# Kernel optimization log

Measured on AMD Instinct MI355X. Metric: run time of the kernel, lower is better.

The kernel has to match this reference:

```python
import jax, jax.numpy as jnp
import numpy as np

B, T, C, HS = 1024, 128, 384, 64


def setup_inputs() -> dict:
    key = jax.random.key(0)
    k1, k2, k3, k4 = jax.random.split(key, 4)
    std = 1.0 / np.sqrt(C)  # ~ nn.Linear default init scale
    return {
        "x": jax.random.normal(k1, (B, T, C), dtype=jnp.float32),
        "Wq": jax.random.normal(k2, (C, HS), dtype=jnp.float32) * std,
        "Wk": jax.random.normal(k3, (C, HS), dtype=jnp.float32) * std,
        "Wv": jax.random.normal(k4, (C, HS), dtype=jnp.float32) * std,
    }


def reference(x, Wq, Wk, Wv):
    # x: [B, T, C]; Wq/Wk/Wv: [C, HS]
    q = jnp.einsum("btc,ch->bth", x, Wq)
    k = jnp.einsum("btc,ch->bth", x, Wk)
    v = jnp.einsum("btc,ch->bth", x, Wv)
    scale = 1.0 / jnp.sqrt(jnp.asarray(k.shape[-1], dtype=x.dtype))
    wei = jnp.einsum("bth,bsh->bts", q, k) * scale  # [B, T, T]
    t = x.shape[1]
    causal = jnp.tril(jnp.ones((t, t), dtype=bool))
    wei = jnp.where(causal, wei, jnp.asarray(-jnp.inf, dtype=wei.dtype))
    wei = jax.nn.softmax(wei, axis=-1)
    # dropout omitted (eval mode / deterministic reference)
    out = jnp.einsum("bts,bsh->bth", wei, v)  # [B, T, HS]
    return out
```

## Files before the change

### kernel.cpp

```cpp
#include <hip/hip_runtime.h>


typedef __attribute__((ext_vector_type(8)))  short  short8;
typedef __attribute__((ext_vector_type(16))) float  floatx16;
typedef __attribute__((ext_vector_type(4)))  float  float4v;

#define T_DIM   128
#define C_DIM   384
#define HS      64
#define NCHUNK  12
#define SLAB    1536

#define QK_PITCH 68
#define V_PITCH  132
#define P_PITCH  132
#define Q_OFF 0
#define K_OFF 17408
#define V_OFF 34816
#define LDS_BYTES 51712
#define P_OFF 0
#define XS_OFF 0
#define XS_BUF 10240
#define XP    80

#define MFMA(a,b,c) __builtin_amdgcn_mfma_f32_32x32x16_bf16((a),(b),(c),0,0,0)

__device__ inline unsigned short f2bf(float f){
    unsigned u = __builtin_bit_cast(unsigned, f);
    u += 0x7FFFu + ((u >> 16) & 1u);
    return (unsigned short)(u >> 16);
}

__device__ inline short8 ld_b64x2(const char* p){
    union { unsigned long long u[2]; short8 s; } r;
    r.u[0] = *(const unsigned long long*)(p);
    r.u[1] = *(const unsigned long long*)(p + 8);
    return r.s;
}

__global__ void prep_wt(const float* __restrict__ Wq, const float* __restrict__ Wk,
                        const float* __restrict__ Wv, unsigned short* __restrict__ wt){
    int idx = blockIdx.x * 256 + threadIdx.x;
    if (idx >= 48 * SLAB) return;
    int slab = idx / SLAB;
    int rem  = idx - slab * SLAB;
    int n = rem >> 3, j = rem & 7;
    int half = slab & 1, ks = (slab >> 1) & 1, c = slab >> 2;
    int kg = c*32 + ks*16 + half*8 + j;
    const float* W = (n < 64) ? Wq : (n < 128) ? Wk : Wv;
    wt[idx] = f2bf(W[kg * HS + (n & 63)]);
}

__launch_bounds__(256, 2)
__global__ void attn_kernel(const float* __restrict__ x,
                            const unsigned short* __restrict__ wtg,
                            float* __restrict__ out){
    __shared__ __align__(16) char smem[LDS_BYTES];
    const int tid  = threadIdx.x;
    const int lane = tid & 63;
    const int wave = tid >> 6;
    const int l31  = lane & 31;
    const int half = lane >> 5;
    const int koff = half * 8;
    const int b    = blockIdx.x;
    const float* xb = x + (size_t)b * (T_DIM * C_DIM);

    const int mpair = wave & 1;
    const int ntri  = wave >> 1;
    const short8* wf = (const short8*)wtg;
    const int nbase = 96 * ntri + l31;

    const int srow  = tid >> 1;
    const int shalf = tid & 1;
    char* const bw0 = smem + XS_OFF + srow * XP + shalf * 32;

    float4v ldreg[2][4];
    auto xload = [&](int c, int s){
        const float4v* g = (const float4v*)(xb + srow * C_DIM + c * 32 + shalf * 16);
        ldreg[s][0] = g[0]; ldreg[s][1] = g[1];
        ldreg[s][2] = g[2]; ldreg[s][3] = g[3];
    };
    auto cw = [&](int s, int sb){
        short8 o0, o1;
        #pragma unroll
        for (int j = 0; j < 8; ++j){
            o0[j] = (short)f2bf(ldreg[s][j >> 2    ][j & 3]);
            o1[j] = (short)f2bf(ldreg[s][(j >> 2)+2][j & 3]);
        }
        char* p = bw0 + sb * XS_BUF;
        *(short8*)(p)      = o0;
        *(short8*)(p + 16) = o1;
    };

    floatx16 acc[6] = {};
    short8 bfr[2][2][3];

    xload(0, 0);
    xload(1, 1);
    #pragma unroll
    for (int ks = 0; ks < 2; ++ks)
        #pragma unroll
        for (int nbl = 0; nbl < 3; ++nbl)
            bfr[0][ks][nbl] = wf[((0*2 + ks)*2 + half)*192 + nbase + 32*nbl];
    cw(0, 0);
    asm volatile("s_waitcnt lgkmcnt(0)" ::: "memory");
    __builtin_amdgcn_s_barrier();
    asm volatile("" ::: "memory");

    #pragma unroll
    for (int c = 0; c < NCHUNK; ++c){
        if (c + 2 < NCHUNK) xload(c + 2, c & 1);
        if (c + 1 < NCHUNK){
            #pragma unroll
            for (int ks = 0; ks < 2; ++ks)
                #pragma unroll
                for (int nbl = 0; nbl < 3; ++nbl)
                    bfr[(c+1)&1][ks][nbl] =
                        wf[(((c+1)*2 + ks)*2 + half)*192 + nbase + 32*nbl];
        }

        const char* sbuf = smem + XS_OFF + (c & 1) * XS_BUF;
        short8 afr[2][2];
        #pragma unroll
        for (int mbl = 0; mbl < 2; ++mbl){
            const int R = 64*mpair + 32*mbl + l31;
            #pragma unroll
            for (int ks = 0; ks < 2; ++ks)
                afr[ks][mbl] = *(const short8*)(sbuf + R * XP + ks*32 + half*16);
        }
        #pragma unroll
        for (int ks = 0; ks < 2; ++ks)
            #pragma unroll
            for (int nbl = 0; nbl < 3; ++nbl){
                acc[nbl*2+0] = MFMA(afr[ks][0], bfr[c&1][ks][nbl], acc[nbl*2+0]);
                acc[nbl*2+1] = MFMA(afr[ks][1], bfr[c&1][ks][nbl], acc[nbl*2+1]);
            }

        if (c + 1 < NCHUNK){
            cw((c+1)&1, (c+1)&1);
            asm volatile("s_waitcnt lgkmcnt(0)" ::: "memory");
            __builtin_amdgcn_s_barrier();
            asm volatile("" ::: "memory");
        }
    }
    __syncthreads();

    const float QSCALE = 0.125f * 1.44269504088896f;
    #pragma unroll
    for (int nbl = 0; nbl < 3; ++nbl)
        #pragma unroll
        for (int mbl = 0; mbl < 2; ++mbl){
            floatx16 A = acc[nbl*2+mbl];
            int nb = 3*ntri + nbl;
            int mb = 2*mpair + mbl;
            if (nb < 4){
                int base  = (nb < 2) ? Q_OFF : K_OFF;
                int col   = 32 * (nb & 1) + l31;
                float sc  = (nb < 2) ? QSCALE : 1.0f;
                char* bp  = smem + base + col * 2;
                #pragma unroll
                for (int r = 0; r < 16; ++r){
                    int t = 32*mb + (r&3) + 8*(r>>2) + 4*half;
                    *(unsigned short*)(bp + t * (QK_PITCH*2)) = f2bf(A[r] * sc);
                }
            } else {
                int h = 32*(nb-4) + l31;
                char* bp = smem + V_OFF + h * (V_PITCH*2);
                #pragma unroll
                for (int g = 0; g < 4; ++g){
                    int t0 = 32*mb + 8*g + 4*half;
                    union { unsigned short s[4]; unsigned long long u; } pk;
                    pk.s[0]=f2bf(A[4*g+0]); pk.s[1]=f2bf(A[4*g+1]);
                    pk.s[2]=f2bf(A[4*g+2]); pk.s[3]=f2bf(A[4*g+3]);
                    *(unsigned long long*)(bp + t0*2) = pk.u;
                }
            }
        }
    __syncthreads();

    floatx16 accS[4] = {};
    #pragma unroll
    for (int ks = 0; ks < 4; ++ks){
        short8 aq = ld_b64x2(smem + Q_OFF + (32*wave + l31)*(QK_PITCH*2) + (ks*16 + koff)*2);
        #pragma unroll
        for (int st = 0; st < 4; ++st)
            if (st <= wave){
                short8 bk = ld_b64x2(smem + K_OFF + (32*st + l31)*(QK_PITCH*2) + (ks*16 + koff)*2);
                accS[st] = MFMA(aq, bk, accS[st]);
            }
    }
    #pragma unroll
    for (int st = 0; st < 4; ++st)
        if (st <= wave){
            #pragma unroll
            for (int r = 0; r < 16; ++r){
                int trow = (r&3) + 8*(r>>2) + 4*half;
                float e = exp2f(accS[st][r]);
                if (st == wave && l31 > trow) e = 0.0f;
                accS[st][r] = e;
            }
        }

    float linv[16];
    #pragma unroll
    for (int r = 0; r < 16; ++r){
        float l = accS[0][r] + accS[1][r] + accS[2][r] + accS[3][r];
        #pragma unroll
        for (int m = 1; m <= 16; m <<= 1)
            l += __shfl_xor(l, m);
        linv[r] = 1.0f / l;
    }
    __syncthreads();

    #pragma unroll
    for (int st = 0; st < 4; ++st)
        if (st <= wave){
            char* bp = smem + P_OFF + (32*st + l31) * 2;
            #pragma unroll
            for (int r = 0; r < 16; ++r){
                int t = 32*wave + (r&3) + 8*(r>>2) + 4*half;
                *(unsigned short*)(bp + t * (P_PITCH*2)) = f2bf(accS[st][r]);
            }
        }
    __syncthreads();

    floatx16 accO0 = {}, accO1 = {};
    const int nks = 2 * (wave + 1);
    #pragma unroll
    for (int ks = 0; ks < 8; ++ks)
        if (ks < nks){
            short8 ap  = ld_b64x2(smem + P_OFF + (32*wave + l31)*(P_PITCH*2) + (ks*16 + koff)*2);
            short8 bv0 = ld_b64x2(smem + V_OFF + l31        *(V_PITCH*2) + (ks*16 + koff)*2);
            short8 bv1 = ld_b64x2(smem + V_OFF + (l31 + 32) *(V_PITCH*2) + (ks*16 + koff)*2);
            accO0 = MFMA(ap, bv0, accO0);
            accO1 = MFMA(ap, bv1, accO1);
        }

    float* ob = out + (size_t)b * (T_DIM * HS);
    #pragma unroll
    for (int r = 0; r < 16; ++r){
        int t = 32*wave + (r&3) + 8*(r>>2) + 4*half;
        ob[t*HS + l31]      = accO0[r] * linv[r];
        ob[t*HS + l31 + 32] = accO1[r] * linv[r];
    }
}

extern "C" void kernel_launch(void* const* d_in, const int* in_sizes, int n_in,
                              void* d_out, int out_size, void* d_ws, size_t ws_size,
                              hipStream_t stream){
    const float* x  = (const float*)d_in[0];
    const float* Wq = (const float*)d_in[1];
    const float* Wk = (const float*)d_in[2];
    const float* Wv = (const float*)d_in[3];
    unsigned short* wt = (unsigned short*)d_ws;

    prep_wt<<<288, 256, 0, stream>>>(Wq, Wk, Wv, wt);
    attn_kernel<<<1024, 256, 0, stream>>>(x, wt, (float*)d_out);
}
```

Before: 304.4 us.

## Double block size to 512 threads and split attention key tiles across wave pairs

The kernel now launches 512 threads per batch, with eight waves instead of four. In the projection GEMM each wave owns one 32-row block instead of two, and each x chunk is staged by four threads per row. In the attention phase, two waves share each query row-tile and take alternating key tiles. Softmax row sums are combined through LDS, and partial outputs are reduced through LDS before the store. This is meant to spread the causal triangle's load more evenly and raise occupancy, at the cost of extra barriers, an LDS reduction and weight fragments no longer being prefetched a chunk ahead.

```diff
diff --git a/kernel.cpp b/kernel.cpp
--- a/kernel.cpp
+++ b/kernel.cpp
@@ -17,8 +17,10 @@
 #define Q_OFF 0
 #define K_OFF 17408
 #define V_OFF 34816
-#define LDS_BYTES 51712
+#define RS_OFF 51712
+#define LDS_BYTES 52736
 #define P_OFF 0
+#define OX_OFF 0
 #define XS_OFF 0
 #define XS_BUF 10240
 #define XP    80
@@ -51,7 +53,7 @@
     wt[idx] = f2bf(W[kg * HS + (n & 63)]);
 }
 
-__launch_bounds__(256, 2)
+__launch_bounds__(512, 4)
 __global__ void attn_kernel(const float* __restrict__ x,
                             const unsigned short* __restrict__ wtg,
                             float* __restrict__ out){
@@ -65,43 +67,42 @@
     const int b    = blockIdx.x;
     const float* xb = x + (size_t)b * (T_DIM * C_DIM);
 
-    const int mpair = wave & 1;
-    const int ntri  = wave >> 1;
+    const int mblk = wave & 3;
+    const int ngrp = wave >> 2;
     const short8* wf = (const short8*)wtg;
-    const int nbase = 96 * ntri + l31;
-
-    const int srow  = tid >> 1;
-    const int shalf = tid & 1;
-    char* const bw0 = smem + XS_OFF + srow * XP + shalf * 32;
-
-    float4v ldreg[2][4];
+    const int nbase = 96 * ngrp + l31;
+
+    const int srow  = tid >> 2;
+    const int spart = tid & 3;
+    char* const bw0 = smem + XS_OFF + srow * XP + spart * 16;
+    const float* const xs0 = xb + srow * C_DIM + spart * 8;
+
+    float4v ldreg[2][2];
     auto xload = [&](int c, int s){
-        const float4v* g = (const float4v*)(xb + srow * C_DIM + c * 32 + shalf * 16);
+        const float4v* g = (const float4v*)(xs0 + c * 32);
         ldreg[s][0] = g[0]; ldreg[s][1] = g[1];
-        ldreg[s][2] = g[2]; ldreg[s][3] = g[3];
     };
     auto cw = [&](int s, int sb){
-        short8 o0, o1;
-        #pragma unroll
-        for (int j = 0; j < 8; ++j){
-            o0[j] = (short)f2bf(ldreg[s][j >> 2    ][j & 3]);
-            o1[j] = (short)f2bf(ldreg[s][(j >> 2)+2][j & 3]);
-        }
-        char* p = bw0 + sb * XS_BUF;
-        *(short8*)(p)      = o0;
-        *(short8*)(p + 16) = o1;
+        short8 o;
+        #pragma unroll
+        for (int j = 0; j < 8; ++j)
+            o[j] = (short)f2bf(ldreg[s][j >> 2][j & 3]);
+        *(short8*)(bw0 + sb * XS_BUF) = o;
     };
 
-    floatx16 acc[6] = {};
-    short8 bfr[2][2][3];
+    floatx16 acc[3] = {};
+    short8 bfr[2][3];
+    auto wload = [&](int c){
+        #pragma unroll
+        for (int ks = 0; ks < 2; ++ks)
+            #pragma unroll
+            for (int nbl = 0; nbl < 3; ++nbl)
+                bfr[ks][nbl] = wf[((c*2 + ks)*2 + half)*192 + nbase + 32*nbl];
+    };
 
     xload(0, 0);
     xload(1, 1);
-    #pragma unroll
-    for (int ks = 0; ks < 2; ++ks)
-        #pragma unroll
-        for (int nbl = 0; nbl < 3; ++nbl)
-            bfr[0][ks][nbl] = wf[((0*2 + ks)*2 + half)*192 + nbase + 32*nbl];
+    wload(0);
     cw(0, 0);
     asm volatile("s_waitcnt lgkmcnt(0)" ::: "memory");
     __builtin_amdgcn_s_barrier();
@@ -110,34 +111,21 @@
     #pragma unroll
     for (int c = 0; c < NCHUNK; ++c){
         if (c + 2 < NCHUNK) xload(c + 2, c & 1);
+        if (c + 1 < NCHUNK) cw((c+1)&1, (c+1)&1);
+
+        const char* sbuf = smem + XS_OFF + (c & 1) * XS_BUF;
+        const int R = 32*mblk + l31;
+        short8 afr0 = *(const short8*)(sbuf + R * XP + 0*32 + half*16);
+        short8 afr1 = *(const short8*)(sbuf + R * XP + 1*32 + half*16);
+        #pragma unroll
+        for (int nbl = 0; nbl < 3; ++nbl)
+            acc[nbl] = MFMA(afr0, bfr[0][nbl], acc[nbl]);
+        #pragma unroll
+        for (int nbl = 0; nbl < 3; ++nbl)
+            acc[nbl] = MFMA(afr1, bfr[1][nbl], acc[nbl]);
+
         if (c + 1 < NCHUNK){
-            #pragma unroll
-            for (int ks = 0; ks < 2; ++ks)
-                #pragma unroll
-                for (int nbl = 0; nbl < 3; ++nbl)
-                    bfr[(c+1)&1][ks][nbl] =
-                        wf[(((c+1)*2 + ks)*2 + half)*192 + nbase + 32*nbl];
-        }
-
-        const char* sbuf = smem + XS_OFF + (c & 1) * XS_BUF;
-        short8 afr[2][2];
-        #pragma unroll
-        for (int mbl = 0; mbl < 2; ++mbl){
-            const int R = 64*mpair + 32*mbl + l31;
-            #pragma unroll
-            for (int ks = 0; ks < 2; ++ks)
-                afr[ks][mbl] = *(const short8*)(sbuf + R * XP + ks*32 + half*16);
-        }
-        #pragma unroll
-        for (int ks = 0; ks < 2; ++ks)
-            #pragma unroll
-            for (int nbl = 0; nbl < 3; ++nbl){
-                acc[nbl*2+0] = MFMA(afr[ks][0], bfr[c&1][ks][nbl], acc[nbl*2+0]);
-                acc[nbl*2+1] = MFMA(afr[ks][1], bfr[c&1][ks][nbl], acc[nbl*2+1]);
-            }
-
-        if (c + 1 < NCHUNK){
-            cw((c+1)&1, (c+1)&1);
+            wload(c + 1);
             asm volatile("s_waitcnt lgkmcnt(0)" ::: "memory");
             __builtin_amdgcn_s_barrier();
             asm volatile("" ::: "memory");
@@ -147,101 +135,147 @@
 
     const float QSCALE = 0.125f * 1.44269504088896f;
     #pragma unroll
-    for (int nbl = 0; nbl < 3; ++nbl)
-        #pragma unroll
-        for (int mbl = 0; mbl < 2; ++mbl){
-            floatx16 A = acc[nbl*2+mbl];
-            int nb = 3*ntri + nbl;
-            int mb = 2*mpair + mbl;
-            if (nb < 4){
-                int base  = (nb < 2) ? Q_OFF : K_OFF;
-                int col   = 32 * (nb & 1) + l31;
-                float sc  = (nb < 2) ? QSCALE : 1.0f;
-                char* bp  = smem + base + col * 2;
-                #pragma unroll
-                for (int r = 0; r < 16; ++r){
-                    int t = 32*mb + (r&3) + 8*(r>>2) + 4*half;
-                    *(unsigned short*)(bp + t * (QK_PITCH*2)) = f2bf(A[r] * sc);
-                }
-            } else {
-                int h = 32*(nb-4) + l31;
-                char* bp = smem + V_OFF + h * (V_PITCH*2);
-                #pragma unroll
-                for (int g = 0; g < 4; ++g){
-                    int t0 = 32*mb + 8*g + 4*half;
-                    union { unsigned short s[4]; unsigned long long u; } pk;
-                    pk.s[0]=f2bf(A[4*g+0]); pk.s[1]=f2bf(A[4*g+1]);
-                    pk.s[2]=f2bf(A[4*g+2]); pk.s[3]=f2bf(A[4*g+3]);
-                    *(unsigned long long*)(bp + t0*2) = pk.u;
-                }
-            }
-        }
-    __syncthreads();
-
-    floatx16 accS[4] = {};
+    for (int nbl = 0; nbl < 3; ++nbl){
+        floatx16 A = acc[nbl];
+        int nb = 3*ngrp + nbl;
+        int mb = mblk;
+        if (nb < 4){
+            int base  = (nb < 2) ? Q_OFF : K_OFF;
+            int col   = 32 * (nb & 1) + l31;
+            float sc  = (nb < 2) ? QSCALE : 1.0f;
+            char* bp  = smem + base + col * 2;
+            #pragma unroll
+            for (int r = 0; r < 16; ++r){
+                int t = 32*mb + (r&3) + 8*(r>>2) + 4*half;
+                *(unsigned short*)(bp + t * (QK_PITCH*2)) = f2bf(A[r] * sc);
+            }
+        } else {
+            int h = 32*(nb-4) + l31;
+            char* bp = smem + V_OFF + h * (V_PITCH*2);
+            #pragma unroll
+            for (int g = 0; g < 4; ++g){
+                int t0 = 32*mb + 8*g + 4*half;
+                union { unsigned short s[4]; unsigned long long u; } pk;
+                pk.s[0]=f2bf(A[4*g+0]); pk.s[1]=f2bf(A[4*g+1]);
+                pk.s[2]=f2bf(A[4*g+2]); pk.s[3]=f2bf(A[4*g+3]);
+                *(unsigned long long*)(bp + t0*2) = pk.u;
+            }
+        }
+    }
+    __syncthreads();
+
+    const int rt = wave & 3;
+    const int cg = wave >> 2;
+    floatx16 accS[2] = {};
     #pragma unroll
     for (int ks = 0; ks < 4; ++ks){
-        short8 aq = ld_b64x2(smem + Q_OFF + (32*wave + l31)*(QK_PITCH*2) + (ks*16 + koff)*2);
-        #pragma unroll
-        for (int st = 0; st < 4; ++st)
-            if (st <= wave){
-                short8 bk = ld_b64x2(smem + K_OFF + (32*st + l31)*(QK_PITCH*2) + (ks*16 + koff)*2);
-                accS[st] = MFMA(aq, bk, accS[st]);
-            }
-    }
-    #pragma unroll
-    for (int st = 0; st < 4; ++st)
-        if (st <= wave){
+        short8 aq = ld_b64x2(smem + Q_OFF + (32*rt + l31)*(QK_PITCH*2) + (ks*16 + koff)*2);
+        #pragma unroll
+        for (int i = 0; i < 2; ++i){
+            int ct = cg + 2*i;
+            if (ct <= rt){
+                short8 bk = ld_b64x2(smem + K_OFF + (32*ct + l31)*(QK_PITCH*2) + (ks*16 + koff)*2);
+                accS[i] = MFMA(aq, bk, accS[i]);
+            }
+        }
+    }
+    #pragma unroll
+    for (int i = 0; i < 2; ++i){
+        int ct = cg + 2*i;
+        if (ct <= rt){
             #pragma unroll
             for (int r = 0; r < 16; ++r){
                 int trow = (r&3) + 8*(r>>2) + 4*half;
-                float e = exp2f(accS[st][r]);
-                if (st == wave && l31 > trow) e = 0.0f;
-                accS[st][r] = e;
-            }
-        }
-
-    float linv[16];
+                float e = exp2f(accS[i][r]);
+                if (ct == rt && l31 > trow) e = 0.0f;
+                accS[i][r] = e;
+            }
+        }
+    }
+
+    float ps[16];
     #pragma unroll
     for (int r = 0; r < 16; ++r){
-        float l = accS[0][r] + accS[1][r] + accS[2][r] + accS[3][r];
+        float l = accS[0][r] + accS[1][r];
         #pragma unroll
         for (int m = 1; m <= 16; m <<= 1)
             l += __shfl_xor(l, m);
-        linv[r] = 1.0f / l;
-    }
-    __syncthreads();
-
-    #pragma unroll
-    for (int st = 0; st < 4; ++st)
-        if (st <= wave){
-            char* bp = smem + P_OFF + (32*st + l31) * 2;
+        ps[r] = l;
+    }
+    __syncthreads();
+
+    #pragma unroll
+    for (int i = 0; i < 2; ++i){
+        int ct = cg + 2*i;
+        if (ct <= rt){
+            char* bp = smem + P_OFF + (32*ct + l31) * 2;
             #pragma unroll
             for (int r = 0; r < 16; ++r){
-                int t = 32*wave + (r&3) + 8*(r>>2) + 4*half;
-                *(unsigned short*)(bp + t * (P_PITCH*2)) = f2bf(accS[st][r]);
-            }
-        }
-    __syncthreads();
+                int t = 32*rt + (r&3) + 8*(r>>2) + 4*half;
+                *(unsigned short*)(bp + t * (P_PITCH*2)) = f2bf(accS[i][r]);
+            }
+        }
+    }
+    if (l31 == 0){
+        #pragma unroll
+        for (int r = 0; r < 16; ++r){
+            int row = (r&3) + 8*(r>>2) + 4*half;
+            *(float*)(smem + RS_OFF + ((rt*2 + cg)*32 + row)*4) = ps[r];
+        }
+    }
+    __syncthreads();
+
+    float linv[16];
+    if (cg){
+        #pragma unroll
+        for (int r = 0; r < 16; ++r){
+            int row = (r&3) + 8*(r>>2) + 4*half;
+            float s0 = *(const float*)(smem + RS_OFF + ((rt*2 + 0)*32 + row)*4);
+            float s1 = *(const float*)(smem + RS_OFF + ((rt*2 + 1)*32 + row)*4);
+            linv[r] = 1.0f / (s0 + s1);
+        }
+    }
 
     floatx16 accO0 = {}, accO1 = {};
-    const int nks = 2 * (wave + 1);
-    #pragma unroll
-    for (int ks = 0; ks < 8; ++ks)
-        if (ks < nks){
-            short8 ap  = ld_b64x2(smem + P_OFF + (32*wave + l31)*(P_PITCH*2) + (ks*16 + koff)*2);
-            short8 bv0 = ld_b64x2(smem + V_OFF + l31        *(V_PITCH*2) + (ks*16 + koff)*2);
-            short8 bv1 = ld_b64x2(smem + V_OFF + (l31 + 32) *(V_PITCH*2) + (ks*16 + koff)*2);
-            accO0 = MFMA(ap, bv0, accO0);
-            accO1 = MFMA(ap, bv1, accO1);
-        }
-
-    float* ob = out + (size_t)b * (T_DIM * HS);
-    #pragma unroll
-    for (int r = 0; r < 16; ++r){
-        int t = 32*wave + (r&3) + 8*(r>>2) + 4*half;
-        ob[t*HS + l31]      = accO0[r] * linv[r];
-        ob[t*HS + l31 + 32] = accO1[r] * linv[r];
+    #pragma unroll
+    for (int i = 0; i < 2; ++i){
+        int ct = cg + 2*i;
+        if (ct <= rt){
+            #pragma unroll
+            for (int kk = 0; kk < 2; ++kk){
+                int ks = 2*ct + kk;
+                short8 ap  = ld_b64x2(smem + P_OFF + (32*rt + l31)*(P_PITCH*2) + (ks*16 + koff)*2);
+                short8 bv0 = ld_b64x2(smem + V_OFF + l31        *(V_PITCH*2) + (ks*16 + koff)*2);
+                short8 bv1 = ld_b64x2(smem + V_OFF + (l31 + 32) *(V_PITCH*2) + (ks*16 + koff)*2);
+                accO0 = MFMA(ap, bv0, accO0);
+                accO1 = MFMA(ap, bv1, accO1);
+            }
+        }
+    }
+    __syncthreads();
+
+    if (cg == 0){
+        char* ox = smem + OX_OFF + rt * 8192;
+        #pragma unroll
+        for (int r = 0; r < 16; ++r){
+            int row = (r&3) + 8*(r>>2) + 4*half;
+            *(float*)(ox + row*256 + l31*4)       = accO0[r];
+            *(float*)(ox + row*256 + 128 + l31*4) = accO1[r];
+        }
+    }
+    __syncthreads();
+    if (cg == 1){
+        const char* ox = smem + OX_OFF + rt * 8192;
+        float* ob = out + (size_t)b * (T_DIM * HS);
+        #pragma unroll
+        for (int r = 0; r < 16; ++r){
+            int row = (r&3) + 8*(r>>2) + 4*half;
+            int t = 32*rt + row;
+            float o0 = *(const float*)(ox + row*256 + l31*4)       + accO0[r];
+            float o1 = *(const float*)(ox + row*256 + 128 + l31*4) + accO1[r];
+            ob[t*HS + l31]      = o0 * linv[r];
+            ob[t*HS + l31 + 32] = o1 * linv[r];
+        }
     }
 }
 
@@ -255,5 +289,5 @@
     unsigned short* wt = (unsigned short*)d_ws;
 
     prep_wt<<<288, 256, 0, stream>>>(Wq, Wk, Wv, wt);
-    attn_kernel<<<1024, 256, 0, stream>>>(x, wt, (float*)d_out);
-}
+    attn_kernel<<<1024, 512, 0, stream>>>(x, wt, (float*)d_out);
+}
```

Result: no change. 307.9 us (+1.2%).
